# Kernel tuning notes

Hardware: AMD Instinct MI355X
Metric: run time of the kernel (lower is better)

Reference implementation:

```python
import jax, jax.numpy as jnp
import numpy as np

N_NODES = 100000
N_EDGES = 1600000
N_CLUSTERS = 1024
EPS = 1e-5


def gcn_conv(x, W, b, src, dst, n, ew=None):
    """PyG GCNConv: symmetric norm with self-loops. ew: optional edge weight/mask."""
    h = x @ W
    if ew is None:
        ew = jnp.ones(src.shape[0], h.dtype)
    deg = jax.ops.segment_sum(ew, dst, num_segments=n) + 1.0  # +1 self loop
    dinv = jax.lax.rsqrt(deg)
    coef = dinv[src] * dinv[dst] * ew  # [E]
    out = jax.ops.segment_sum(h[src] * coef[:, None], dst, num_segments=n)
    out = out + h * (dinv * dinv)[:, None]  # self-loop messages
    return out + b


def instance_norm(x):
    # PyG InstanceNorm, batch=None -> single graph, no affine, biased variance
    mu = jnp.mean(x, axis=0, keepdims=True)
    var = jnp.mean((x - mu) ** 2, axis=0, keepdims=True)
    return (x - mu) * jax.lax.rsqrt(var + EPS)


def forward(x, WG1, bG1, WfG1, bfG1, WG2, bG2, WfG2, bfG2,
            WL1, bL1, WfL1, bfL1, WL2, bL2, WfL2, bfL2,
            WO1, bO1, WfO1, bfO1, WO2, bO2, WfO2, bfO2, WO3, bO3, WfO3, bfO3,
            adj, in_batch, cluster):
    elu = jax.nn.elu
    n = x.shape[0]
    src, dst = adj[0], adj[1]
    # global GCN stack
    h = elu(gcn_conv(x, WG1, bG1, src, dst, n))
    h = elu(h @ WfG1 + bfG1)
    h = elu(gcn_conv(h, WG2, bG2, src, dst, n))
    h = elu(h @ WfG2 + bfG2)
    y = instance_norm(h)  # [N, 256]
    # avg_pool over clusters (single graph -> batch offset is 0 but kept faithful)
    bc = cluster + in_batch * N_CLUSTERS  # [N]
    cnt = jax.ops.segment_sum(jnp.ones(n, y.dtype), bc, num_segments=N_CLUSTERS)
    px = jax.ops.segment_sum(y, bc, num_segments=N_CLUSTERS) / jnp.maximum(cnt, 1.0)[:, None]
    # pool edges: map through cluster, remove self-loops, coalesce (dedupe via sort+mask)
    psrc, pdst = bc[src], bc[dst]
    key = psrc * N_CLUSTERS + pdst
    order = jnp.argsort(key)
    ks = key[order]
    s2, d2 = psrc[order], pdst[order]
    first = jnp.concatenate([jnp.ones((1,), bool), ks[1:] != ks[:-1]])
    emask = (first & (s2 != d2)).astype(y.dtype)
    # local GCN stack on compressed graph
    lx = elu(gcn_conv(px, WL1, bL1, s2, d2, N_CLUSTERS, emask))
    lx = elu(lx @ WfL1 + bfL1)
    lx = elu(gcn_conv(lx, WL2, bL2, s2, d2, N_CLUSTERS, emask))
    lx = elu(lx @ WfL2 + bfL2)  # [C, 64]
    # gather-broadcast compressed features back to nodes
    comp = lx[bc]  # [N, 64]
    z = jnp.concatenate([y, comp], axis=1)  # [N, 320]
    z = elu(gcn_conv(z, WO1, bO1, src, dst, n))
    z = elu(z @ WfO1 + bfO1)
    z = elu(gcn_conv(z, WO2, bO2, src, dst, n))
    z = elu(z @ WfO2 + bfO2)
    z = elu(gcn_conv(z, WO3, bO3, src, dst, n))
    z = elu(z @ WfO3 + bfO3)
    return z


def _lin(key, i, o):
    k1, k2 = jax.random.split(key)
    s = 1.0 / np.sqrt(i)
    return (jax.random.normal(k1, (i, o), jnp.float32) * s,
            jax.random.normal(k2, (o,), jnp.float32) * s)


def setup_inputs() -> dict:
    key = jax.random.key(0)
    ks = jax.random.split(key, 20)
    inp = {}
    inp['x'] = jax.random.normal(ks[0], (N_NODES, 3), jnp.float32)
    inp['adj'] = jax.random.randint(ks[1], (2, N_EDGES), 0, N_NODES, jnp.int64 if jax.config.jax_enable_x64 else jnp.int32)
    inp['num_graphs'] = 1
    inp['in_batch'] = jnp.zeros((N_NODES,), jnp.int32)
    inp['cluster'] = jax.random.randint(ks[2], (N_NODES,), 0, N_CLUSTERS, jnp.int32)
    dims = [('G1', 3, 64), ('fG1', 64, 64), ('G2', 64, 256), ('fG2', 256, 256),
            ('L1', 256, 128), ('fL1', 128, 128), ('L2', 128, 64), ('fL2', 64, 64),
            ('O1', 320, 128), ('fO1', 128, 128), ('O2', 128, 32), ('fO2', 32, 32),
            ('O3', 32, 3), ('fO3', 3, 3)]
    for j, (name, i, o) in enumerate(dims):
        W, b = _lin(ks[3 + j], i, o)
        inp['W' + name] = W
        inp['b' + name] = b
    return inp


def reference(x, adj, num_graphs, in_batch, cluster,
              WG1, bG1, WfG1, bfG1, WG2, bG2, WfG2, bfG2,
              WL1, bL1, WfL1, bfL1, WL2, bL2, WfL2, bfL2,
              WO1, bO1, WfO1, bfO1, WO2, bO2, WfO2, bfO2, WO3, bO3, WfO3, bfO3):
    return forward(x, WG1, bG1, WfG1, bfG1, WG2, bG2, WfG2, bfG2,
                   WL1, bL1, WfL1, bfL1, WL2, bL2, WfL2, bfL2,
                   WO1, bO1, WfO1, bfO1, WO2, bO2, WfO2, bfO2,
                   WO3, bO3, WfO3, bfO3, adj, in_batch, cluster)
```

## Files before the change

### kernel.cpp

```cpp
#include <hip/hip_runtime.h>


#define NCLUST 1024

typedef short bf16x8 __attribute__((ext_vector_type(8)));
typedef float f32x4 __attribute__((ext_vector_type(4)));

__device__ __forceinline__ float elu1(float x) { return x > 0.f ? x : expm1f(x); }

__device__ __forceinline__ unsigned f2bf(float f) {
    union { float f; unsigned u; } c; c.f = f;
    unsigned u = c.u;
    return (u + 0x7fffu + ((u >> 16) & 1u)) >> 16;
}
__device__ __forceinline__ float bf2f(unsigned h) {
    union { unsigned u; float f; } c; c.u = h << 16; return c.f;
}

union U8 { unsigned u[4]; bf16x8 v; };

__device__ __forceinline__ void wpack_body(const float* W, unsigned* Phi, unsigned* Plo,
                                           int K, int BN, int t) {
    int NT = BN / 16;
    int lane = t & 63;
    int rest = t >> 6;
    int ct = rest % NT;
    int s = rest / NT;
    int col = ct * 16 + (lane & 15);
    int g = lane >> 4;
    int k0 = s * 32;
    float e[8];
#pragma unroll
    for (int j = 0; j < 4; j++) {
        e[j]     = W[(size_t)(k0 + 4 * g + j) * BN + col];
        e[4 + j] = W[(size_t)(k0 + 16 + 4 * g + j) * BN + col];
    }
#pragma unroll
    for (int j = 0; j < 4; j++) {
        unsigned h0 = f2bf(e[2 * j]), h1 = f2bf(e[2 * j + 1]);
        Phi[(size_t)t * 4 + j] = h0 | (h1 << 16);
        unsigned l0 = f2bf(e[2 * j] - bf2f(h0));
        unsigned l1 = f2bf(e[2 * j + 1] - bf2f(h1));
        Plo[(size_t)t * 4 + j] = l0 | (l1 << 16);
    }
}

struct PackDesc { const float* W; unsigned* Ph; unsigned* Pl; int K, BN, tbase; };
struct InitArgs {
    PackDesc d[6]; int tot;
    int4* z1; int nz1; int4* z2; int nz2;
};

__global__ void k_init(InitArgs a) {
    int t = blockIdx.x * 256 + threadIdx.x;
    if (t < a.nz1) a.z1[t] = make_int4(0, 0, 0, 0);
    else if (t - a.nz1 < a.nz2) a.z2[t - a.nz1] = make_int4(0, 0, 0, 0);
    if (t < a.tot) {
        int i = 0;
#pragma unroll
        for (int j = 1; j < 6; j++) if (t >= a.d[j].tbase) i = j;
        wpack_body(a.d[i].W, a.d[i].Ph, a.d[i].Pl, a.d[i].K, a.d[i].BN,
                   t - a.d[i].tbase);
    }
}

__global__ void k_hist(const int* __restrict__ key, int* __restrict__ deg, int E) {
    int e = blockIdx.x * 256 + threadIdx.x;
    if (e < E) atomicAdd(&deg[key[e]], 1);
}

__global__ void k_scan_block(const int* __restrict__ deg, int* __restrict__ rowptr,
                             int* __restrict__ bsum, int n) {
    __shared__ int lds[256];
    int tid = threadIdx.x;
    int base = blockIdx.x * 1024 + tid * 4;
    int v0 = base + 0 < n ? deg[base + 0] : 0;
    int v1 = base + 1 < n ? deg[base + 1] : 0;
    int v2 = base + 2 < n ? deg[base + 2] : 0;
    int v3 = base + 3 < n ? deg[base + 3] : 0;
    int tsum = v0 + v1 + v2 + v3;
    lds[tid] = tsum; __syncthreads();
    for (int off = 1; off < 256; off <<= 1) {
        int t = (tid >= off) ? lds[tid - off] : 0;
        __syncthreads();
        lds[tid] += t;
        __syncthreads();
    }
    int run = lds[tid] - tsum;
    if (base + 0 < n) rowptr[base + 0] = run; run += v0;
    if (base + 1 < n) rowptr[base + 1] = run; run += v1;
    if (base + 2 < n) rowptr[base + 2] = run; run += v2;
    if (base + 3 < n) rowptr[base + 3] = run;
    if (tid == 255) bsum[blockIdx.x] = lds[255];
}

__global__ void k_nodeinit(int* __restrict__ rowptr, const int* __restrict__ bsum,
                           const int* __restrict__ deg, const int* __restrict__ cluster,
                           const int* __restrict__ inb, float* __restrict__ dinv,
                           int* __restrict__ bc, int* __restrict__ cdeg, int n, int nb) {
    __shared__ int pfx[128];
    int tid = threadIdx.x;
    if (tid < 128) pfx[tid] = (tid < nb) ? bsum[tid] : 0;
    __syncthreads();
    for (int off = 1; off < 128; off <<= 1) {
        int v = 0;
        if (tid < 128 && tid >= off) v = pfx[tid - off];
        __syncthreads();
        if (tid < 128) pfx[tid] += v;
        __syncthreads();
    }
    int i = blockIdx.x * 256 + tid;
    if (i >= n) return;
    int j = i >> 10;
    int base = (j == 0) ? 0 : pfx[j - 1];
    rowptr[i] += base;
    dinv[i] = rsqrtf((float)deg[i] + 1.0f);
    int c = cluster[i] + inb[i] * NCLUST;
    bc[i] = c;
    atomicAdd(&cdeg[c], 1);
}

__global__ void k_fillc(const int* __restrict__ src, const int* __restrict__ dst,
                        const float* __restrict__ dinv, const int* __restrict__ rowptr,
                        int* __restrict__ fill, int2* __restrict__ csr_ev, int E,
                        const int* __restrict__ bc, const int* __restrict__ crowptr,
                        int* __restrict__ cfill, int* __restrict__ cnodes, int n) {
    int e = blockIdx.x * 256 + threadIdx.x;
    if (e < E) {
        int d = dst[e];
        int pos = rowptr[d] + atomicAdd(&fill[d], 1);
        int s = src[e];
        csr_ev[pos] = make_int2(s, __float_as_int(dinv[s]));
    }
    if (e < n) {
        int c = bc[e];
        int pos = crowptr[c] + atomicAdd(&cfill[c], 1);
        cnodes[pos] = e;
    }
}

template <int F, int OB>
__global__ __launch_bounds__(256) void k_prop4sb(
        const unsigned short* __restrict__ hbf, const float* __restrict__ dinv,
        const int* __restrict__ rowptr, const int* __restrict__ deg,
        const int2* __restrict__ csr_ev,
        const float* __restrict__ bias, float* __restrict__ outf,
        unsigned short* __restrict__ outb, int n, int flags) {
    constexpr int FS = F / 4;
    constexpr int ES = 64 / FS;
    const int node = (blockIdx.x * 256 + threadIdx.x) >> 6;
    if (node >= n) return;
    const int l = threadIdx.x & 63;
    const int fs = l & (FS - 1);
    const int ep = l / FS;
    const int fi = fs * 4;
    const int start = rowptr[node];
    const int cnt = deg[node];
    float ax = 0.f, ay = 0.f, az = 0.f, aw = 0.f;
    for (int j = ep; j < cnt; j += ES) {
        const int2 ev = csr_ev[start + j];
        int s = ev.x;
        float w = __int_as_float(ev.y);
        const ushort4 v = *reinterpret_cast<const ushort4*>(&hbf[(size_t)s * F + fi]);
        ax += w * bf2f(v.x); ay += w * bf2f(v.y);
        az += w * bf2f(v.z); aw += w * bf2f(v.w);
    }
#pragma unroll
    for (int off = FS; off < 64; off <<= 1) {
        ax += __shfl_xor(ax, off);
        ay += __shfl_xor(ay, off);
        az += __shfl_xor(az, off);
        aw += __shfl_xor(aw, off);
    }
    if (ep == 0) {
        float di = dinv[node];
        const ushort4 sv = *reinterpret_cast<const ushort4*>(&hbf[(size_t)node * F + fi]);
        float4 o;
        o.x = di * ax + di * di * bf2f(sv.x);
        o.y = di * ay + di * di * bf2f(sv.y);
        o.z = di * az + di * di * bf2f(sv.z);
        o.w = di * aw + di * di * bf2f(sv.w);
        if (flags) {
            const float4 b = *reinterpret_cast<const float4*>(&bias[fi]);
            o.x = elu1(o.x + b.x); o.y = elu1(o.y + b.y);
            o.z = elu1(o.z + b.z); o.w = elu1(o.w + b.w);
        }
        if constexpr (OB) {
            ushort4 ob;
            ob.x = (unsigned short)f2bf(o.x); ob.y = (unsigned short)f2bf(o.y);
            ob.z = (unsigned short)f2bf(o.z); ob.w = (unsigned short)f2bf(o.w);
            *reinterpret_cast<ushort4*>(&outb[(size_t)node * F + fi]) = ob;
        } else {
            *reinterpret_cast<float4*>(&outf[(size_t)node * F + fi]) = o;
        }
    }
}

__global__ void k_prop3f1(const float* __restrict__ h, const float* __restrict__ dinv,
                          const int* __restrict__ rowptr, const int* __restrict__ deg,
                          const int2* __restrict__ csr_ev,
                          const float* __restrict__ WG1, const float* __restrict__ bG1,
                          unsigned short* __restrict__ outb, int n) {
    int node = blockIdx.x * 256 + threadIdx.x;
    if (node >= n) return;
    int start = rowptr[node], cnt = deg[node];
    float a0 = 0.f, a1 = 0.f, a2 = 0.f;
    for (int j = 0; j < cnt; j++) {
        const int2 ev = csr_ev[start + j];
        int s = ev.x;
        float w = __int_as_float(ev.y);
        a0 += w * h[(size_t)s * 3 + 0];
        a1 += w * h[(size_t)s * 3 + 1];
        a2 += w * h[(size_t)s * 3 + 2];
    }
    float di = dinv[node];
    float p0 = di * a0 + di * di * h[(size_t)node * 3 + 0];
    float p1 = di * a1 + di * di * h[(size_t)node * 3 + 1];
    float p2 = di * a2 + di * di * h[(size_t)node * 3 + 2];
    unsigned short* op = outb + (size_t)node * 64;
#pragma unroll 4
    for (int c = 0; c < 64; c += 4) {
        ushort4 ob;
        ob.x = (unsigned short)f2bf(elu1(p0 * WG1[c + 0] + p1 * WG1[64 + c + 0] + p2 * WG1[128 + c + 0] + bG1[c + 0]));
        ob.y = (unsigned short)f2bf(elu1(p0 * WG1[c + 1] + p1 * WG1[64 + c + 1] + p2 * WG1[128 + c + 1] + bG1[c + 1]));
        ob.z = (unsigned short)f2bf(elu1(p0 * WG1[c + 2] + p1 * WG1[64 + c + 2] + p2 * WG1[128 + c + 2] + bG1[c + 2]));
        ob.w = (unsigned short)f2bf(elu1(p0 * WG1[c + 3] + p1 * WG1[64 + c + 3] + p2 * WG1[128 + c + 3] + bG1[c + 3]));
        *reinterpret_cast<ushort4*>(op + c) = ob;
    }
}

__global__ void k_prop3out(const float* __restrict__ h, const float* __restrict__ dinv,
                           const int* __restrict__ rowptr, const int* __restrict__ deg,
                           const int2* __restrict__ csr_ev,
                           const float* __restrict__ bO3, const float* __restrict__ WfO3,
                           const float* __restrict__ bfO3, float* __restrict__ out, int n) {
    int node = blockIdx.x * 256 + threadIdx.x;
    if (node >= n) return;
    int start = rowptr[node], cnt = deg[node];
    float a0 = 0.f, a1 = 0.f, a2 = 0.f;
    for (int j = 0; j < cnt; j++) {
        const int2 ev = csr_ev[start + j];
        int s = ev.x;
        float w = __int_as_float(ev.y);
        a0 += w * h[(size_t)s * 3 + 0];
        a1 += w * h[(size_t)s * 3 + 1];
        a2 += w * h[(size_t)s * 3 + 2];
    }
    float di = dinv[node];
    float o0 = elu1(di * a0 + di * di * h[(size_t)node * 3 + 0] + bO3[0]);
    float o1 = elu1(di * a1 + di * di * h[(size_t)node * 3 + 1] + bO3[1]);
    float o2 = elu1(di * a2 + di * di * h[(size_t)node * 3 + 2] + bO3[2]);
#pragma unroll
    for (int c = 0; c < 3; c++) {
        out[(size_t)node * 3 + c] =
            elu1(o0 * WfO3[c] + o1 * WfO3[3 + c] + o2 * WfO3[6 + c] + bfO3[c]);
    }
}

__global__ void k_normprep(const float* __restrict__ W, const float* __restrict__ insum,
                           const float* __restrict__ insumsq, unsigned* __restrict__ Phi,
                           unsigned* __restrict__ Plo, float* __restrict__ corr,
                           float* __restrict__ mu, float* __restrict__ rstd, int n) {
    const float fn = (float)n;
    const int bid = blockIdx.x, tid = threadIdx.x;
    if (bid == 16) {
        float m = insum[tid] / fn;
        float var = insumsq[tid] / fn - m * m;
        mu[tid] = m;
        rstd[tid] = rsqrtf(var + 1e-5f);
        return;
    }
    {
        int t = bid * 256 + tid;
        int lane = t & 63, rest = t >> 6;
        int ct = rest % 8, s = rest / 8;
        int col = ct * 16 + (lane & 15);
        int g = lane >> 4;
        int k0 = s * 32;
        float e[8];
#pragma unroll
        for (int j = 0; j < 4; j++) {
            int ka = k0 + 4 * g + j;
            int kb = k0 + 16 + 4 * g + j;
            float ma = insum[ka] / fn;
            float sa = rsqrtf(insumsq[ka] / fn - ma * ma + 1e-5f);
            float mb = insum[kb] / fn;
            float sb = rsqrtf(insumsq[kb] / fn - mb * mb + 1e-5f);
            e[j]     = W[(size_t)ka * 128 + col] * sa;
            e[4 + j] = W[(size_t)kb * 128 + col] * sb;
        }
#pragma unroll
        for (int j = 0; j < 4; j++) {
            unsigned h0 = f2bf(e[2 * j]), h1 = f2bf(e[2 * j + 1]);
            Phi[(size_t)t * 4 + j] = h0 | (h1 << 16);
            unsigned l0 = f2bf(e[2 * j] - bf2f(h0));
            unsigned l1 = f2bf(e[2 * j + 1] - bf2f(h1));
            Plo[(size_t)t * 4 + j] = l0 | (l1 << 16);
        }
    }
    if (tid < 128) {
        int k0 = bid * 16;
        float s = 0.f;
        for (int k = k0; k < k0 + 16; k++) {
            float m = insum[k] / fn;
            float r = rsqrtf(insumsq[k] / fn - m * m + 1e-5f);
            s += m * r * W[(size_t)k * 128 + tid];
        }
        atomicAdd(&corr[tid], s);
    }
}

template <int BN, bool ABF, int WAVES>
__global__ __launch_bounds__(WAVES * 64) void k_gmfma(
        const float* __restrict__ A, const unsigned short* __restrict__ Abf,
        const unsigned* __restrict__ Phi, const unsigned* __restrict__ Plo,
        const float* __restrict__ bias, const float* __restrict__ sub,
        const float* __restrict__ add, const int* __restrict__ addidx,
        float* __restrict__ C, unsigned short* __restrict__ Cbf,
        int N, int K, int flags) {
    constexpr int NT = BN / 16;
    constexpr int WCOL = (BN == 256) ? 4 : (BN == 128 ? 2 : 1);
    constexpr int WROW = WAVES / WCOL;
    constexpr int NTW = NT / WCOL;
    constexpr int BR = 32 * WROW;
    const int t = threadIdx.x;
    const int w = t >> 6, l = t & 63;
    const int wr = w / WCOL, wc = w % WCOL;
    const int l15 = l & 15, g = l >> 4;
    const int row0 = blockIdx.x * BR + wr * 32;
    const int ctbase = wc * NTW;
    int ar0 = row0 + l15;      ar0 = ar0 < N ? ar0 : N - 1;
    int ar1 = row0 + 16 + l15; ar1 = ar1 < N ? ar1 : N - 1;
    const float* ap0 = ABF ? nullptr : A + (size_t)ar0 * K;
    const float* ap1 = ABF ? nullptr : A + (size_t)ar1 * K;
    const unsigned short* ab0 = ABF ? Abf + (size_t)ar0 * K : nullptr;
    const unsigned short* ab1 = ABF ? Abf + (size_t)ar1 * K : nullptr;

    f32x4 acc[2][NTW];
#pragma unroll
    for (int f = 0; f < 2; f++)
#pragma unroll
        for (int ct = 0; ct < NTW; ct++) acc[f][ct] = (f32x4){0.f, 0.f, 0.f, 0.f};

    auto loadW = [&](int s, U8* wh, U8* wl) {
        const unsigned* pb = Phi + ((size_t)(s * NT + ctbase) * 64 + l) * 4;
        const unsigned* pl = Plo + ((size_t)(s * NT + ctbase) * 64 + l) * 4;
#pragma unroll
        for (int ct = 0; ct < NTW; ct++) {
            wh[ct] = *reinterpret_cast<const U8*>(pb + (size_t)ct * 256);
            wl[ct] = *reinterpret_cast<const U8*>(pl + (size_t)ct * 256);
        }
    };
    auto loadA = [&](int s, U8* ahi, U8* alo) {
        const int k0 = s * 32;
        if constexpr (ABF) {
#pragma unroll
            for (int f = 0; f < 2; f++) {
                const unsigned short* ab = f ? ab1 : ab0;
                const uint2 hA = *reinterpret_cast<const uint2*>(ab + k0 + 4 * g);
                const uint2 hB = *reinterpret_cast<const uint2*>(ab + k0 + 16 + 4 * g);
                ahi[f].u[0] = hA.x; ahi[f].u[1] = hA.y;
                ahi[f].u[2] = hB.x; ahi[f].u[3] = hB.y;
            }
        } else {
#pragma unroll
            for (int f = 0; f < 2; f++) {
                const float* ap = f ? ap1 : ap0;
                const float4 a0 = *reinterpret_cast<const float4*>(ap + k0 + 4 * g);
                const float4 a1 = *reinterpret_cast<const float4*>(ap + k0 + 16 + 4 * g);
                float e[8] = {a0.x, a0.y, a0.z, a0.w, a1.x, a1.y, a1.z, a1.w};
#pragma unroll
                for (int j = 0; j < 4; j++) {
                    unsigned h0 = f2bf(e[2 * j]), h1 = f2bf(e[2 * j + 1]);
                    ahi[f].u[j] = h0 | (h1 << 16);
                    unsigned l0 = f2bf(e[2 * j] - bf2f(h0));
                    unsigned l1 = f2bf(e[2 * j + 1] - bf2f(h1));
                    alo[f].u[j] = l0 | (l1 << 16);
                }
            }
        }
    };
    auto domfma = [&](U8* wh, U8* wl, U8* ahi, U8* alo) {
#pragma unroll
        for (int ct = 0; ct < NTW; ct++) {
            acc[0][ct] = __builtin_amdgcn_mfma_f32_16x16x32_bf16(ahi[0].v, wh[ct].v, acc[0][ct], 0, 0, 0);
            acc[0][ct] = __builtin_amdgcn_mfma_f32_16x16x32_bf16(ahi[0].v, wl[ct].v, acc[0][ct], 0, 0, 0);
            acc[1][ct] = __builtin_amdgcn_mfma_f32_16x16x32_bf16(ahi[1].v, wh[ct].v, acc[1][ct], 0, 0, 0);
            acc[1][ct] = __builtin_amdgcn_mfma_f32_16x16x32_bf16(ahi[1].v, wl[ct].v, acc[1][ct], 0, 0, 0);
            if constexpr (!ABF) {
                acc[0][ct] = __builtin_amdgcn_mfma_f32_16x16x32_bf16(alo[0].v, wh[ct].v, acc[0][ct], 0, 0, 0);
                acc[1][ct] = __builtin_amdgcn_mfma_f32_16x16x32_bf16(alo[1].v, wh[ct].v, acc[1][ct], 0, 0, 0);
            }
        }
    };

    U8 whA[NTW], wlA[NTW], ahiA[2], aloA[2];
    U8 whB[NTW], wlB[NTW], ahiB[2], aloB[2];
    const int nk = K / 32;
    loadW(0, whA, wlA);
    loadA(0, ahiA, aloA);
    int s = 0;
    while (true) {
        const bool hasB = (s + 1 < nk);
        if (hasB) { loadW(s + 1, whB, wlB); loadA(s + 1, ahiB, aloB); }
        domfma(whA, wlA, ahiA, aloA);
        if (!hasB) break;
        const bool hasA2 = (s + 2 < nk);
        if (hasA2) { loadW(s + 2, whA, wlA); loadA(s + 2, ahiA, aloA); }
        domfma(whB, wlB, ahiB, aloB);
        if (!hasA2) break;
        s += 2;
    }
    __syncthreads();
#pragma unroll
    for (int f = 0; f < 2; f++) {
#pragma unroll
        for (int r = 0; r < 4; r++) {
            int row = row0 + 16 * f + 4 * g + r;
            if (row >= N) continue;
            int gi = (add != nullptr) ? addidx[row] : 0;
#pragma unroll
            for (int ct = 0; ct < NTW; ct++) {
                int col = (ctbase + ct) * 16 + l15;
                float o = acc[f][ct][r];
                if (add != nullptr) o += add[(size_t)gi * BN + col];
                if (sub != nullptr) o -= sub[col];
                if (flags) o = elu1(o + bias[col]);
                if (C != nullptr) C[(size_t)row * BN + col] = o;
                if (Cbf != nullptr) Cbf[(size_t)row * BN + col] = (unsigned short)f2bf(o);
            }
        }
    }
}

template <int M, int RPT>
__global__ __launch_bounds__(256) void k_fc(
        const float* __restrict__ A, const float* __restrict__ W,
        const float* __restrict__ bias, const float* __restrict__ add,
        const int* __restrict__ addidx, float* __restrict__ C,
        int N, int K, int flags) {
    constexpr int TX = M / 4;
    constexpr int TY = 256 / TX;
    constexpr int RB = TY * RPT;
    int tx = threadIdx.x % TX;
    int ty = threadIdx.x / TX;
    int row0 = blockIdx.x * RB + ty * RPT;
    float4 acc[RPT];
#pragma unroll
    for (int r = 0; r < RPT; r++) acc[r] = make_float4(0.f, 0.f, 0.f, 0.f);
    for (int k = 0; k < K; k++) {
        float4 w = *reinterpret_cast<const float4*>(&W[(size_t)k * M + tx * 4]);
#pragma unroll
        for (int r = 0; r < RPT; r++) {
            int row = row0 + r;
            row = row < N ? row : N - 1;
            float a = A[(size_t)row * K + k];
            acc[r].x += a * w.x; acc[r].y += a * w.y;
            acc[r].z += a * w.z; acc[r].w += a * w.w;
        }
    }
    if (add != nullptr) {
#pragma unroll
        for (int r = 0; r < RPT; r++) {
            int row = row0 + r;
            if (row < N) {
                int g = addidx[row];
                const float4 v = *reinterpret_cast<const float4*>(&add[(size_t)g * M + tx * 4]);
                acc[r].x += v.x; acc[r].y += v.y; acc[r].z += v.z; acc[r].w += v.w;
            }
        }
    }
    __syncthreads();
    float4 b = make_float4(0.f, 0.f, 0.f, 0.f);
    if (flags) b = *reinterpret_cast<const float4*>(&bias[tx * 4]);
#pragma unroll
    for (int r = 0; r < RPT; r++) {
        int row = row0 + r;
        if (row >= N) break;
        float4 o = acc[r];
        o.x += b.x; o.y += b.y; o.z += b.z; o.w += b.w;
        if (flags) { o.x = elu1(o.x); o.y = elu1(o.y); o.z = elu1(o.z); o.w = elu1(o.w); }
        *reinterpret_cast<float4*>(&C[(size_t)row * M + tx * 4]) = o;
    }
}

__global__ __launch_bounds__(256) void k_fcl2(
        const float* __restrict__ A, const float* __restrict__ W1,
        const float* __restrict__ b1, const float* __restrict__ W2,
        float* __restrict__ lxout, float* __restrict__ compO) {
    __shared__ float lx[32][64];
    const int tid = threadIdx.x;
    const int tx = tid % 16, ty = tid / 16;
    const int row0b = blockIdx.x * 32;
    float4 acc[2];
    acc[0] = make_float4(0.f, 0.f, 0.f, 0.f);
    acc[1] = make_float4(0.f, 0.f, 0.f, 0.f);
    for (int k = 0; k < 64; k++) {
        float4 w = *reinterpret_cast<const float4*>(&W1[(size_t)k * 64 + tx * 4]);
#pragma unroll
        for (int r = 0; r < 2; r++) {
            float a = A[(size_t)(row0b + ty * 2 + r) * 64 + k];
            acc[r].x += a * w.x; acc[r].y += a * w.y;
            acc[r].z += a * w.z; acc[r].w += a * w.w;
        }
    }
    float4 b = *reinterpret_cast<const float4*>(&b1[tx * 4]);
#pragma unroll
    for (int r = 0; r < 2; r++) {
        int lr = ty * 2 + r;
        float4 o;
        o.x = elu1(acc[r].x + b.x); o.y = elu1(acc[r].y + b.y);
        o.z = elu1(acc[r].z + b.z); o.w = elu1(acc[r].w + b.w);
        *reinterpret_cast<float4*>(&lxout[(size_t)(row0b + lr) * 64 + tx * 4]) = o;
        lx[lr][tx * 4 + 0] = o.x; lx[lr][tx * 4 + 1] = o.y;
        lx[lr][tx * 4 + 2] = o.z; lx[lr][tx * 4 + 3] = o.w;
    }
    __syncthreads();
    for (int o = tid; o < 32 * 128; o += 256) {
        int r = o >> 7, c = o & 127;
        float s = 0.f;
        for (int k = 0; k < 64; k++) s += lx[r][k] * W2[(size_t)k * 128 + c];
        compO[(size_t)(row0b + r) * 128 + c] = s;
    }
}

__global__ void k_fc3(const float* __restrict__ A, const float* __restrict__ W,
                      const float* __restrict__ b, float* __restrict__ C,
                      int n, int K, int flags) {
    int r = blockIdx.x * 256 + threadIdx.x;
    if (r >= n) return;
    float a0 = 0.f, a1 = 0.f, a2 = 0.f;
    for (int k = 0; k < K; k++) {
        float a = A[(size_t)r * K + k];
        a0 += a * W[k * 3 + 0]; a1 += a * W[k * 3 + 1]; a2 += a * W[k * 3 + 2];
    }
    if (flags) {
        a0 = elu1(a0 + b[0]); a1 = elu1(a1 + b[1]); a2 = elu1(a2 + b[2]);
    }
    C[(size_t)r * 3 + 0] = a0;
    C[(size_t)r * 3 + 1] = a1;
    C[(size_t)r * 3 + 2] = a2;
}

__global__ void k_instats(const unsigned short* __restrict__ h, float* __restrict__ sum,
                          float* __restrict__ sumsq, int n) {
    int c = threadIdx.x;
    int r0 = blockIdx.x * 128;
    int r1 = r0 + 128 < n ? r0 + 128 : n;
    float s = 0.f, q = 0.f;
    for (int r = r0; r < r1; r++) {
        float v = bf2f(h[(size_t)r * 256 + c]);
        s += v; q += v * v;
    }
    atomicAdd(&sum[c], s);
    atomicAdd(&sumsq[c], q);
}

__global__ __launch_bounds__(256) void k_poolmerge(
        const unsigned short* __restrict__ xh, const int* __restrict__ crowptr,
        const int* __restrict__ cdeg, const int* __restrict__ cnodes,
        const float* __restrict__ mu, const float* __restrict__ rstd,
        float* __restrict__ px,
        const int* __restrict__ src, const int* __restrict__ dst,
        const int* __restrict__ bc, unsigned char* __restrict__ bmT, int E) {
    int bid = blockIdx.x;
    if (bid < NCLUST) {
        int cl = bid;
        int c  = threadIdx.x;
        int start = crowptr[cl];
        int cnt = cdeg[cl];
        float acc = 0.f;
        for (int j = 0; j < cnt; j++) {
            int node = cnodes[start + j];
            acc += bf2f(xh[(size_t)node * 256 + c]);
        }
        float res = acc / fmaxf((float)cnt, 1.0f);
        res = (cnt > 0) ? (res - mu[c]) * rstd[c] : 0.f;
        px[(size_t)cl * 256 + c] = res;
    } else {
        int e = (bid - NCLUST) * 256 + threadIdx.x;
        if (e < E) {
            int ps = bc[src[e]];
            int pd = bc[dst[e]];
            bmT[(size_t)pd * NCLUST + ps] = 1;
        }
    }
}

__global__ __launch_bounds__(256) void k_pooldeg(
        const unsigned char* __restrict__ bmT, float* __restrict__ dinvp) {
    int d = blockIdx.x;
    int t = threadIdx.x;
    const unsigned int v = reinterpret_cast<const unsigned int*>(bmT + (size_t)d * NCLUST)[t];
    int s = (v & 0xff) + ((v >> 8) & 0xff) + ((v >> 16) & 0xff) + ((v >> 24) & 0xff);
    if (t == (d >> 2)) s -= (v >> ((d & 3) * 8)) & 0xff;
    __shared__ int red[256];
    red[t] = s; __syncthreads();
    for (int o = 128; o > 0; o >>= 1) {
        if (t < o) red[t] += red[t + o];
        __syncthreads();
    }
    if (t == 0) dinvp[d] = rsqrtf((float)red[0] + 1.0f);
}

template <int F>
__global__ __launch_bounds__(1024) void k_proppool2(
        const float* __restrict__ h, const float* __restrict__ dinvp,
        const unsigned char* __restrict__ bmT, const float* __restrict__ bias,
        float* __restrict__ out) {
    constexpr int SG = 1024 / F;
    const int d = blockIdx.x;
    const int t = threadIdx.x;
    const int f = t & (F - 1);
    const int sg = t / F;
    const unsigned char* bmrow = bmT + (size_t)d * NCLUST;
    float acc = 0.f;
#pragma unroll 4
    for (int s = sg; s < NCLUST; s += SG) {
        float m = (s != d) ? (float)bmrow[s] : 0.f;
        acc += m * dinvp[s] * h[(size_t)s * F + f];
    }
    __shared__ float red[1024];
    red[t] = acc; __syncthreads();
#pragma unroll
    for (int o = SG / 2; o > 0; o >>= 1) {
        if (sg < o) red[t] += red[t + o * F];
        __syncthreads();
    }
    if (sg == 0) {
        float di = dinvp[d];
        float r = di * red[f] + di * di * h[(size_t)d * F + f] + bias[f];
        out[(size_t)d * F + f] = elu1(r);
    }
}

extern "C" void kernel_launch(void* const* d_in, const int* in_sizes, int n_in,
                              void* d_out, int out_size, void* d_ws, size_t ws_size,
                              hipStream_t stream) {
    const float* x       = (const float*)d_in[0];
    const int*   adj     = (const int*)d_in[1];
    const int*   inb     = (const int*)d_in[3];
    const int*   cluster = (const int*)d_in[4];
    const float* WG1  = (const float*)d_in[5];   const float* bG1  = (const float*)d_in[6];
    const float* WfG1 = (const float*)d_in[7];   const float* bfG1 = (const float*)d_in[8];
    const float* WG2  = (const float*)d_in[9];   const float* bG2  = (const float*)d_in[10];
    const float* WfG2 = (const float*)d_in[11];  const float* bfG2 = (const float*)d_in[12];
    const float* WL1  = (const float*)d_in[13];  const float* bL1  = (const float*)d_in[14];
    const float* WfL1 = (const float*)d_in[15];  const float* bfL1 = (const float*)d_in[16];
    const float* WL2  = (const float*)d_in[17];  const float* bL2  = (const float*)d_in[18];
    const float* WfL2 = (const float*)d_in[19];  const float* bfL2 = (const float*)d_in[20];
    const float* WO1  = (const float*)d_in[21];  const float* bO1  = (const float*)d_in[22];
    const float* WfO1 = (const float*)d_in[23];  const float* bfO1 = (const float*)d_in[24];
    const float* WO2  = (const float*)d_in[25];  const float* bO2  = (const float*)d_in[26];
    const float* WfO2 = (const float*)d_in[27];  const float* bfO2 = (const float*)d_in[28];
    const float* WO3  = (const float*)d_in[29];  const float* bO3  = (const float*)d_in[30];
    const float* WfO3 = (const float*)d_in[31];  const float* bfO3 = (const float*)d_in[32];
    float* out = (float*)d_out;

    const int n = in_sizes[0] / 3;
    const int E = in_sizes[1] / 2;
    const int* src = adj;
    const int* dst = adj + E;

    char* ws = (char*)d_ws;
    size_t off = 0;
    auto alloc = [&](size_t bytes) -> void* {
        void* p = ws + off;
        off = (off + bytes + 255) & ~(size_t)255;
        return p;
    };
    int*   deg     = (int*)alloc((size_t)n * 4);
    int*   fill    = (int*)alloc((size_t)n * 4);
    int*   cdeg    = (int*)alloc(NCLUST * 4);
    int*   cfill   = (int*)alloc(NCLUST * 4);
    int*   rowptr  = (int*)alloc((size_t)n * 4);
    int*   crowptr = (int*)alloc(NCLUST * 4);
    int*   cnodes  = (int*)alloc((size_t)n * 4);
    int*   bcarr   = (int*)alloc((size_t)n * 4);
    float* dinv    = (float*)alloc((size_t)n * 4);
    int*   bsum    = (int*)alloc(512);
    int2*  csr_ev  = (int2*)alloc((size_t)E * 8);
    float* X       = (float*)alloc((size_t)n * 256 * 4);
    unsigned short* Xh = (unsigned short*)alloc((size_t)n * 256 * 2);
    float* B       = (float*)alloc((size_t)n * 128 * 4);
    unsigned short* Bh = (unsigned short*)alloc((size_t)n * 128 * 2);
    float* insum   = (float*)alloc(256 * 4);
    float* insumsq = (float*)alloc(256 * 4);
    float* px      = (float*)alloc((size_t)NCLUST * 256 * 4);
    unsigned char* bmT = (unsigned char*)alloc((size_t)NCLUST * NCLUST);
    float* corr    = (float*)alloc(128 * 4);
    float* mu      = (float*)alloc(256 * 4);
    float* rstd    = (float*)alloc(256 * 4);
    float* dinvp   = (float*)alloc(NCLUST * 4);
    float* lA      = (float*)alloc((size_t)NCLUST * 128 * 4);
    float* lB      = (float*)alloc((size_t)NCLUST * 128 * 4);
    unsigned* pfG1h = (unsigned*)alloc(2048 * 4);   unsigned* pfG1l = (unsigned*)alloc(2048 * 4);
    unsigned* pG2h  = (unsigned*)alloc(8192 * 4);   unsigned* pG2l  = (unsigned*)alloc(8192 * 4);
    unsigned* pfG2h = (unsigned*)alloc(32768 * 4);  unsigned* pfG2l = (unsigned*)alloc(32768 * 4);
    unsigned* pO1h  = (unsigned*)alloc(16384 * 4);  unsigned* pO1l  = (unsigned*)alloc(16384 * 4);
    unsigned* pfO1h = (unsigned*)alloc(8192 * 4);   unsigned* pfO1l = (unsigned*)alloc(8192 * 4);
    unsigned* pO2h  = (unsigned*)alloc(2048 * 4);   unsigned* pO2l  = (unsigned*)alloc(2048 * 4);
    unsigned* pfO2h = (unsigned*)alloc(512 * 4);    unsigned* pfO2l = (unsigned*)alloc(512 * 4);
    (void)ws_size; (void)n_in; (void)out_size;

    unsigned short* Bh1 = Bh;
    unsigned short* Bh2 = Bh + (size_t)n * 64;

    auto cdiv = [](int a, int b) { return (a + b - 1) / b; };
    const int EB = cdiv(E, 256);
    const int PB = cdiv(n, 4);

    int nz1 = (int)(((char*)rowptr - (char*)deg) / 16);
    int nz2 = (int)(((char*)mu - (char*)insum) / 16);
    InitArgs ia;
    ia.d[0] = {WfG1, pfG1h, pfG1l, 64, 64, 0};
    ia.d[1] = {WG2,  pG2h,  pG2l,  64, 256, 512};
    ia.d[2] = {WfG2, pfG2h, pfG2l, 256, 256, 2560};
    ia.d[3] = {WfO1, pfO1h, pfO1l, 128, 128, 10752};
    ia.d[4] = {WO2,  pO2h,  pO2l,  128, 32, 12800};
    ia.d[5] = {WfO2, pfO2h, pfO2l, 32, 32, 13312};
    ia.tot = 13440;
    ia.z1 = (int4*)deg; ia.nz1 = nz1;
    ia.z2 = (int4*)insum; ia.nz2 = nz2;
    int initN = (nz1 + nz2 > ia.tot) ? (nz1 + nz2) : ia.tot;
    k_init<<<cdiv(initN, 256), 256, 0, stream>>>(ia);

    k_hist<<<EB, 256, 0, stream>>>(dst, deg, E);
    int nb = cdiv(n, 1024);
    k_scan_block<<<nb, 256, 0, stream>>>(deg, rowptr, bsum, n);
    k_nodeinit<<<cdiv(n, 256), 256, 0, stream>>>(rowptr, bsum, deg, cluster, inb,
                                                 dinv, bcarr, cdeg, n, nb);
    k_scan_block<<<1, 256, 0, stream>>>(cdeg, crowptr, bsum, NCLUST);
    k_fillc<<<EB, 256, 0, stream>>>(src, dst, dinv, rowptr, fill, csr_ev, E,
                                    bcarr, crowptr, cfill, cnodes, n);

    k_prop3f1<<<cdiv(n, 256), 256, 0, stream>>>(x, dinv, rowptr, deg, csr_ev,
                                                WG1, bG1, Bh1, n);
    k_gmfma<64, true, 8><<<cdiv(n, 256), 512, 0, stream>>>(nullptr, Bh1, pfG1h, pfG1l, bfG1,
                                                           nullptr, nullptr, nullptr,
                                                           nullptr, Bh1, n, 64, 1);
    k_prop4sb<64, 1><<<PB, 256, 0, stream>>>(Bh1, dinv, rowptr, deg, csr_ev,
                                             nullptr, nullptr, Bh2, n, 0);
    k_gmfma<256, true, 8><<<cdiv(n, 64), 512, 0, stream>>>(nullptr, Bh2, pG2h, pG2l, bG2,
                                                           nullptr, nullptr, nullptr,
                                                           nullptr, Xh, n, 64, 1);
    k_gmfma<256, true, 8><<<cdiv(n, 64), 512, 0, stream>>>(nullptr, Xh, pfG2h, pfG2l, bfG2,
                                                           nullptr, nullptr, nullptr,
                                                           nullptr, Xh, n, 256, 1);

    k_instats<<<cdiv(n, 128), 256, 0, stream>>>(Xh, insum, insumsq, n);
    k_normprep<<<17, 256, 0, stream>>>(WO1, insum, insumsq, pO1h, pO1l, corr, mu, rstd, n);

    k_poolmerge<<<NCLUST + EB, 256, 0, stream>>>(Xh, crowptr, cdeg, cnodes, mu, rstd, px,
                                                 src, dst, bcarr, bmT, E);
    k_pooldeg<<<NCLUST, 256, 0, stream>>>(bmT, dinvp);

    k_fc<128, 2><<<cdiv(NCLUST, 16), 256, 0, stream>>>(px, WL1, nullptr, nullptr, nullptr,
                                                       lA, NCLUST, 256, 0);
    k_proppool2<128><<<NCLUST, 1024, 0, stream>>>(lA, dinvp, bmT, bL1, lB);
    k_fc<128, 2><<<cdiv(NCLUST, 16), 256, 0, stream>>>(lB, WfL1, bfL1, nullptr, nullptr,
                                                       lA, NCLUST, 128, 1);
    k_fc<64, 2><<<cdiv(NCLUST, 32), 256, 0, stream>>>(lA, WL2, nullptr, nullptr, nullptr,
                                                      lB, NCLUST, 128, 0);
    k_proppool2<64><<<NCLUST, 1024, 0, stream>>>(lB, dinvp, bmT, bL2, lA);
    k_fcl2<<<NCLUST / 32, 256, 0, stream>>>(lA, WfL2, bfL2, WO1 + (size_t)256 * 128,
                                            lB, lA);

    k_gmfma<128, true, 8><<<cdiv(n, 128), 512, 0, stream>>>(nullptr, Xh, pO1h, pO1l, nullptr,
                                                            corr, lA, bcarr, nullptr, Bh,
                                                            n, 256, 0);
    k_prop4sb<128, 1><<<PB, 256, 0, stream>>>(Bh, dinv, rowptr, deg, csr_ev,
                                              bO1, nullptr, Xh, n, 1);
    k_gmfma<128, true, 8><<<cdiv(n, 128), 512, 0, stream>>>(nullptr, Xh, pfO1h, pfO1l, bfO1,
                                                            nullptr, nullptr, nullptr,
                                                            nullptr, Xh, n, 128, 1);
    k_gmfma<32, true, 8><<<cdiv(n, 256), 512, 0, stream>>>(nullptr, Xh, pO2h, pO2l, nullptr,
                                                           nullptr, nullptr, nullptr,
                                                           nullptr, Bh, n, 128, 0);
    k_prop4sb<32, 1><<<PB, 256, 0, stream>>>(Bh, dinv, rowptr, deg, csr_ev,
                                             bO2, nullptr, Xh, n, 1);
    k_gmfma<32, true, 8><<<cdiv(n, 256), 512, 0, stream>>>(nullptr, Xh, pfO2h, pfO2l, bfO2,
                                                           nullptr, nullptr, nullptr,
                                                           X, nullptr, n, 32, 1);
    k_fc3<<<cdiv(n, 256), 256, 0, stream>>>(X, WO3, nullptr, B, n, 32, 0);
    k_prop3out<<<cdiv(n, 256), 256, 0, stream>>>(B, dinv, rowptr, deg, csr_ev,
                                                 bO3, WfO3, bfO3, out, n);
}
```

Before: 1.190 ms.

## Stage packed GEMM weights through LDS with async double-buffered global_load_lds

For GEMM widths of 128 and above, the packed hi/lo bf16 weight tiles are now staged cooperatively into a double-buffered LDS area using global_load_lds, and each wave reads its tiles from LDS. Before, every wave loaded the same weight tiles straight from global memory into registers. This is meant to cut redundant global/L2 weight traffic and register pressure, at the cost of a block-wide barrier per K step and extra LDS use. The unused fp32-A input path (ABF=false) is removed, and the template is simplified to match.

```diff
diff --git a/kernel.cpp b/kernel.cpp
--- a/kernel.cpp
+++ b/kernel.cpp
@@ -310,9 +310,9 @@
     }
 }
 
-template <int BN, bool ABF, int WAVES>
+template <int BN, int WAVES>
 __global__ __launch_bounds__(WAVES * 64) void k_gmfma(
-        const float* __restrict__ A, const unsigned short* __restrict__ Abf,
+        const unsigned short* __restrict__ Abf,
         const unsigned* __restrict__ Phi, const unsigned* __restrict__ Plo,
         const float* __restrict__ bias, const float* __restrict__ sub,
         const float* __restrict__ add, const int* __restrict__ addidx,
@@ -323,6 +323,8 @@
     constexpr int WROW = WAVES / WCOL;
     constexpr int NTW = NT / WCOL;
     constexpr int BR = 32 * WROW;
+    constexpr bool LDSW = (BN >= 128);
+    __shared__ unsigned lds_w[LDSW ? 2 * 2 * NT * 256 : 1];
     const int t = threadIdx.x;
     const int w = t >> 6, l = t & 63;
     const int wr = w / WCOL, wc = w % WCOL;
@@ -331,10 +333,8 @@
     const int ctbase = wc * NTW;
     int ar0 = row0 + l15;      ar0 = ar0 < N ? ar0 : N - 1;
     int ar1 = row0 + 16 + l15; ar1 = ar1 < N ? ar1 : N - 1;
-    const float* ap0 = ABF ? nullptr : A + (size_t)ar0 * K;
-    const float* ap1 = ABF ? nullptr : A + (size_t)ar1 * K;
-    const unsigned short* ab0 = ABF ? Abf + (size_t)ar0 * K : nullptr;
-    const unsigned short* ab1 = ABF ? Abf + (size_t)ar1 * K : nullptr;
+    const unsigned short* ab0 = Abf + (size_t)ar0 * K;
+    const unsigned short* ab1 = Abf + (size_t)ar1 * K;
 
     f32x4 acc[2][NTW];
 #pragma unroll
@@ -342,76 +342,101 @@
 #pragma unroll
         for (int ct = 0; ct < NTW; ct++) acc[f][ct] = (f32x4){0.f, 0.f, 0.f, 0.f};
 
-    auto loadW = [&](int s, U8* wh, U8* wl) {
-        const unsigned* pb = Phi + ((size_t)(s * NT + ctbase) * 64 + l) * 4;
-        const unsigned* pl = Plo + ((size_t)(s * NT + ctbase) * 64 + l) * 4;
-#pragma unroll
-        for (int ct = 0; ct < NTW; ct++) {
-            wh[ct] = *reinterpret_cast<const U8*>(pb + (size_t)ct * 256);
-            wl[ct] = *reinterpret_cast<const U8*>(pl + (size_t)ct * 256);
+    auto loadA = [&](int s, U8* ahi) {
+        const int k0 = s * 32;
+#pragma unroll
+        for (int f = 0; f < 2; f++) {
+            const unsigned short* ab = f ? ab1 : ab0;
+            const uint2 hA = *reinterpret_cast<const uint2*>(ab + k0 + 4 * g);
+            const uint2 hB = *reinterpret_cast<const uint2*>(ab + k0 + 16 + 4 * g);
+            ahi[f].u[0] = hA.x; ahi[f].u[1] = hA.y;
+            ahi[f].u[2] = hB.x; ahi[f].u[3] = hB.y;
         }
     };
-    auto loadA = [&](int s, U8* ahi, U8* alo) {
-        const int k0 = s * 32;
-        if constexpr (ABF) {
-#pragma unroll
-            for (int f = 0; f < 2; f++) {
-                const unsigned short* ab = f ? ab1 : ab0;
-                const uint2 hA = *reinterpret_cast<const uint2*>(ab + k0 + 4 * g);
-                const uint2 hB = *reinterpret_cast<const uint2*>(ab + k0 + 16 + 4 * g);
-                ahi[f].u[0] = hA.x; ahi[f].u[1] = hA.y;
-                ahi[f].u[2] = hB.x; ahi[f].u[3] = hB.y;
-            }
-        } else {
-#pragma unroll
-            for (int f = 0; f < 2; f++) {
-                const float* ap = f ? ap1 : ap0;
-                const float4 a0 = *reinterpret_cast<const float4*>(ap + k0 + 4 * g);
-                const float4 a1 = *reinterpret_cast<const float4*>(ap + k0 + 16 + 4 * g);
-                float e[8] = {a0.x, a0.y, a0.z, a0.w, a1.x, a1.y, a1.z, a1.w};
-#pragma unroll
-                for (int j = 0; j < 4; j++) {
-                    unsigned h0 = f2bf(e[2 * j]), h1 = f2bf(e[2 * j + 1]);
-                    ahi[f].u[j] = h0 | (h1 << 16);
-                    unsigned l0 = f2bf(e[2 * j] - bf2f(h0));
-                    unsigned l1 = f2bf(e[2 * j + 1] - bf2f(h1));
-                    alo[f].u[j] = l0 | (l1 << 16);
-                }
-            }
-        }
-    };
-    auto domfma = [&](U8* wh, U8* wl, U8* ahi, U8* alo) {
+    auto domfma = [&](U8* wh, U8* wl, U8* ahi) {
 #pragma unroll
         for (int ct = 0; ct < NTW; ct++) {
             acc[0][ct] = __builtin_amdgcn_mfma_f32_16x16x32_bf16(ahi[0].v, wh[ct].v, acc[0][ct], 0, 0, 0);
             acc[0][ct] = __builtin_amdgcn_mfma_f32_16x16x32_bf16(ahi[0].v, wl[ct].v, acc[0][ct], 0, 0, 0);
             acc[1][ct] = __builtin_amdgcn_mfma_f32_16x16x32_bf16(ahi[1].v, wh[ct].v, acc[1][ct], 0, 0, 0);
             acc[1][ct] = __builtin_amdgcn_mfma_f32_16x16x32_bf16(ahi[1].v, wl[ct].v, acc[1][ct], 0, 0, 0);
-            if constexpr (!ABF) {
-                acc[0][ct] = __builtin_amdgcn_mfma_f32_16x16x32_bf16(alo[0].v, wh[ct].v, acc[0][ct], 0, 0, 0);
-                acc[1][ct] = __builtin_amdgcn_mfma_f32_16x16x32_bf16(alo[1].v, wh[ct].v, acc[1][ct], 0, 0, 0);
+        }
+    };
+
+    const int nk = K / 32;
+
+    if constexpr (LDSW) {
+        auto stage = [&](int s, int b) {
+            unsigned* base = lds_w + (size_t)b * (2 * NT * 256);
+            for (int i = w; i < 2 * NT; i += WAVES) {
+                const unsigned* gsrc = (i < NT)
+                    ? Phi + (size_t)(s * NT + i) * 256 + l * 4
+                    : Plo + (size_t)(s * NT + (i - NT)) * 256 + l * 4;
+                __builtin_amdgcn_global_load_lds(
+                    (const __attribute__((address_space(1))) unsigned*)gsrc,
+                    (__attribute__((address_space(3))) unsigned*)(base + i * 256),
+                    16, 0, 0);
             }
-        }
-    };
-
-    U8 whA[NTW], wlA[NTW], ahiA[2], aloA[2];
-    U8 whB[NTW], wlB[NTW], ahiB[2], aloB[2];
-    const int nk = K / 32;
-    loadW(0, whA, wlA);
-    loadA(0, ahiA, aloA);
-    int s = 0;
-    while (true) {
-        const bool hasB = (s + 1 < nk);
-        if (hasB) { loadW(s + 1, whB, wlB); loadA(s + 1, ahiB, aloB); }
-        domfma(whA, wlA, ahiA, aloA);
-        if (!hasB) break;
-        const bool hasA2 = (s + 2 < nk);
-        if (hasA2) { loadW(s + 2, whA, wlA); loadA(s + 2, ahiA, aloA); }
-        domfma(whB, wlB, ahiB, aloB);
-        if (!hasA2) break;
-        s += 2;
-    }
-    __syncthreads();
+        };
+        auto loadWlds = [&](int b, U8* wh, U8* wl) {
+            const unsigned* base = lds_w + (size_t)b * (2 * NT * 256);
+#pragma unroll
+            for (int ct = 0; ct < NTW; ct++) {
+                wh[ct] = *reinterpret_cast<const U8*>(base + (ctbase + ct) * 256 + l * 4);
+                wl[ct] = *reinterpret_cast<const U8*>(base + (NT + ctbase + ct) * 256 + l * 4);
+            }
+        };
+
+        U8 wh[NTW], wl[NTW], ahiA[2], ahiB[2];
+        stage(0, 0);
+        loadA(0, ahiA);
+        __syncthreads();
+        int s = 0;
+        while (true) {
+            const bool hasB = (s + 1 < nk);
+            if (hasB) { stage(s + 1, (s + 1) & 1); loadA(s + 1, ahiB); }
+            loadWlds(s & 1, wh, wl);
+            domfma(wh, wl, ahiA);
+            __syncthreads();
+            if (!hasB) break;
+            s++;
+            const bool hasA2 = (s + 1 < nk);
+            if (hasA2) { stage(s + 1, (s + 1) & 1); loadA(s + 1, ahiA); }
+            loadWlds(s & 1, wh, wl);
+            domfma(wh, wl, ahiB);
+            __syncthreads();
+            if (!hasA2) break;
+            s++;
+        }
+    } else {
+        auto loadW = [&](int s, U8* wh, U8* wl) {
+            const unsigned* pb = Phi + ((size_t)(s * NT + ctbase) * 64 + l) * 4;
+            const unsigned* pl = Plo + ((size_t)(s * NT + ctbase) * 64 + l) * 4;
+#pragma unroll
+            for (int ct = 0; ct < NTW; ct++) {
+                wh[ct] = *reinterpret_cast<const U8*>(pb + (size_t)ct * 256);
+                wl[ct] = *reinterpret_cast<const U8*>(pl + (size_t)ct * 256);
+            }
+        };
+        U8 whA[NTW], wlA[NTW], ahiA[2];
+        U8 whB[NTW], wlB[NTW], ahiB[2];
+        loadW(0, whA, wlA);
+        loadA(0, ahiA);
+        int s = 0;
+        while (true) {
+            const bool hasB = (s + 1 < nk);
+            if (hasB) { loadW(s + 1, whB, wlB); loadA(s + 1, ahiB); }
+            domfma(whA, wlA, ahiA);
+            if (!hasB) break;
+            const bool hasA2 = (s + 2 < nk);
+            if (hasA2) { loadW(s + 2, whA, wlA); loadA(s + 2, ahiA); }
+            domfma(whB, wlB, ahiB);
+            if (!hasA2) break;
+            s += 2;
+        }
+        __syncthreads();
+    }
+
 #pragma unroll
     for (int f = 0; f < 2; f++) {
 #pragma unroll
@@ -736,17 +761,17 @@
 
     k_prop3f1<<<cdiv(n, 256), 256, 0, stream>>>(x, dinv, rowptr, deg, csr_ev,
                                                 WG1, bG1, Bh1, n);
-    k_gmfma<64, true, 8><<<cdiv(n, 256), 512, 0, stream>>>(nullptr, Bh1, pfG1h, pfG1l, bfG1,
-                                                           nullptr, nullptr, nullptr,
-                                                           nullptr, Bh1, n, 64, 1);
+    k_gmfma<64, 8><<<cdiv(n, 256), 512, 0, stream>>>(Bh1, pfG1h, pfG1l, bfG1,
+                                                     nullptr, nullptr, nullptr,
+                                                     nullptr, Bh1, n, 64, 1);
     k_prop4sb<64, 1><<<PB, 256, 0, stream>>>(Bh1, dinv, rowptr, deg, csr_ev,
                                              nullptr, nullptr, Bh2, n, 0);
-    k_gmfma<256, true, 8><<<cdiv(n, 64), 512, 0, stream>>>(nullptr, Bh2, pG2h, pG2l, bG2,
-                                                           nullptr, nullptr, nullptr,
-                                                           nullptr, Xh, n, 64, 1);
-    k_gmfma<256, true, 8><<<cdiv(n, 64), 512, 0, stream>>>(nullptr, Xh, pfG2h, pfG2l, bfG2,
-                                                           nullptr, nullptr, nullptr,
-                                                           nullptr, Xh, n, 256, 1);
+    k_gmfma<256, 8><<<cdiv(n, 64), 512, 0, stream>>>(Bh2, pG2h, pG2l, bG2,
+                                                     nullptr, nullptr, nullptr,
+                                                     nullptr, Xh, n, 64, 1);
+    k_gmfma<256, 8><<<cdiv(n, 64), 512, 0, stream>>>(Xh, pfG2h, pfG2l, bfG2,
+                                                     nullptr, nullptr, nullptr,
+                                                     nullptr, Xh, n, 256, 1);
 
     k_instats<<<cdiv(n, 128), 256, 0, stream>>>(Xh, insum, insumsq, n);
     k_normprep<<<17, 256, 0, stream>>>(WO1, insum, insumsq, pO1h, pO1l, corr, mu, rstd, n);
@@ -766,22 +791,22 @@
     k_fcl2<<<NCLUST / 32, 256, 0, stream>>>(lA, WfL2, bfL2, WO1 + (size_t)256 * 128,
                                             lB, lA);
 
-    k_gmfma<128, true, 8><<<cdiv(n, 128), 512, 0, stream>>>(nullptr, Xh, pO1h, pO1l, nullptr,
-                                                            corr, lA, bcarr, nullptr, Bh,
-                                                            n, 256, 0);
+    k_gmfma<128, 8><<<cdiv(n, 128), 512, 0, stream>>>(Xh, pO1h, pO1l, nullptr,
+                                                      corr, lA, bcarr, nullptr, Bh,
+                                                      n, 256, 0);
     k_prop4sb<128, 1><<<PB, 256, 0, stream>>>(Bh, dinv, rowptr, deg, csr_ev,
                                               bO1, nullptr, Xh, n, 1);
-    k_gmfma<128, true, 8><<<cdiv(n, 128), 512, 0, stream>>>(nullptr, Xh, pfO1h, pfO1l, bfO1,
-                                                            nullptr, nullptr, nullptr,
-                                                            nullptr, Xh, n, 128, 1);
-    k_gmfma<32, true, 8><<<cdiv(n, 256), 512, 0, stream>>>(nullptr, Xh, pO2h, pO2l, nullptr,
-                                                           nullptr, nullptr, nullptr,
-                                                           nullptr, Bh, n, 128, 0);
+    k_gmfma<128, 8><<<cdiv(n, 128), 512, 0, stream>>>(Xh, pfO1h, pfO1l, bfO1,
+                                                      nullptr, nullptr, nullptr,
+                                                      nullptr, Xh, n, 128, 1);
+    k_gmfma<32, 8><<<cdiv(n, 256), 512, 0, stream>>>(Xh, pO2h, pO2l, nullptr,
+                                                     nullptr, nullptr, nullptr,
+                                                     nullptr, Bh, n, 128, 0);
     k_prop4sb<32, 1><<<PB, 256, 0, stream>>>(Bh, dinv, rowptr, deg, csr_ev,
                                              bO2, nullptr, Xh, n, 1);
-    k_gmfma<32, true, 8><<<cdiv(n, 256), 512, 0, stream>>>(nullptr, Xh, pfO2h, pfO2l, bfO2,
-                                                           nullptr, nullptr, nullptr,
-                                                           X, nullptr, n, 32, 1);
+    k_gmfma<32, 8><<<cdiv(n, 256), 512, 0, stream>>>(Xh, pfO2h, pfO2l, bfO2,
+                                                     nullptr, nullptr, nullptr,
+                                                     X, nullptr, n, 32, 1);
     k_fc3<<<cdiv(n, 256), 256, 0, stream>>>(X, WO3, nullptr, B, n, 32, 0);
     k_prop3out<<<cdiv(n, 256), 256, 0, stream>>>(B, dinv, rowptr, deg, csr_ev,
                                                  bO3, WfO3, bfO3, out, n);
```

New measurement: 1.171 ms. About the same (-1.6%).
